# Performance work log

Hardware: AMD Instinct MI355X
Metric: run time of the kernel (lower is better)

The kernel has to match this reference:

```python
import jax, jax.numpy as jnp
import numpy as np
import math

N, C, H = 2048, 256, 8
D = C // H
T, R, E = 8, 12, 32768
BUCKETS = 21
SEED = 128


def _layernorm(x, g, b, eps=1e-5):
    mu = jnp.mean(x, axis=-1, keepdims=True)
    var = jnp.var(x, axis=-1, keepdims=True)
    return (x - mu) * jax.lax.rsqrt(var + eps) * g + b


def _bucketize_dt(dt, num_buckets):
    eps = 1e-06
    signed_log = jnp.sign(dt) * jnp.log1p(jnp.abs(dt) + eps)
    min_v, max_v = -5.0, 5.0
    norm = (jnp.clip(signed_log, min_v, max_v) - min_v) / (max_v - min_v + 1e-09)
    idx = jnp.floor(norm * (num_buckets - 1)).astype(jnp.int32)
    return jnp.clip(idx, 0, num_buckets - 1)


def setup_inputs() -> dict:
    key = jax.random.key(0)
    ks = jax.random.split(key, 24)
    s = 0.02
    inp = {
        'X': jax.random.normal(ks[0], (N, C), jnp.float32),
        'token_type': jax.random.randint(ks[1], (N,), 0, T, jnp.int32),
        'edge_src': jax.random.randint(ks[2], (E,), 0, N, jnp.int32),
        'edge_dst': jax.random.randint(ks[3], (E,), 0, N, jnp.int32),
        'edge_rel': jax.random.randint(ks[4], (E,), 0, R, jnp.int32),
        'time_vec': jax.random.normal(ks[5], (N,), jnp.float32),
        'seed_count': SEED,
        'Wq': jax.random.normal(ks[6], (C, C), jnp.float32) * s,
        'bq': jnp.zeros((C,), jnp.float32),
        'Wk': jax.random.normal(ks[7], (C, C), jnp.float32) * s,
        'bk': jnp.zeros((C,), jnp.float32),
        'Wv': jax.random.normal(ks[8], (C, C), jnp.float32) * s,
        'bv': jnp.zeros((C,), jnp.float32),
        'Wo': jax.random.normal(ks[9], (C, C), jnp.float32) * s,
        'bo': jnp.zeros((C,), jnp.float32),
        'ln1_g': jnp.ones((C,), jnp.float32),
        'ln1_b': jnp.zeros((C,), jnp.float32),
        'ln2_g': jnp.ones((C,), jnp.float32),
        'ln2_b': jnp.zeros((C,), jnp.float32),
        'W1': jax.random.normal(ks[10], (C, 4 * C), jnp.float32) * s,
        'b1': jnp.zeros((4 * C,), jnp.float32),
        'W2': jax.random.normal(ks[11], (4 * C, C), jnp.float32) * s,
        'b2': jnp.zeros((C,), jnp.float32),
        'adj_rel_bias': jnp.zeros((R, H), jnp.float32),
        'typepair_bias': jnp.zeros((T, T, H), jnp.float32),
        'temp_bias': jax.random.normal(ks[12], (BUCKETS, H), jnp.float32) * s,
    }
    return inp


def reference(X, token_type, edge_src, edge_dst, edge_rel, time_vec, seed_count,
              Wq, bq, Wk, bk, Wv, bv, Wo, bo,
              ln1_g, ln1_b, ln2_g, ln2_b, W1, b1, W2, b2,
              adj_rel_bias, typepair_bias, temp_bias):
    n = X.shape[0]
    h = _layernorm(X, ln1_g, ln1_b)
    q = (h @ Wq + bq).reshape(n, H, D)
    k = (h @ Wk + bk).reshape(n, H, D)
    v = (h @ Wv + bv).reshape(n, H, D)
    scores = jnp.einsum('nhd,mhd->hnm', q, k) / math.sqrt(D)  # [H, N, N]

    # structural bias, factored as [N, N, H] then transposed
    bias = typepair_bias[token_type][:, token_type]            # [N, N, H]
    bias = bias.at[edge_src, edge_dst].add(adj_rel_bias[edge_rel])
    # seed-wise temporal bias on the first seed_count rows
    dt = time_vec[None, :] - time_vec[:seed_count, None]       # [S, N]
    tb = temp_bias[_bucketize_dt(dt, BUCKETS)]                 # [S, N, H]
    bias = bias.at[:seed_count].add(tb)

    attn = jax.nn.softmax(scores + bias.transpose(2, 0, 1), axis=-1)
    o = jnp.einsum('hnm,mhd->nhd', attn, v).reshape(n, C)
    x = X + (o @ Wo + bo)

    h2 = _layernorm(x, ln2_g, ln2_b)
    f = jax.nn.gelu(h2 @ W1 + b1, approximate=False) @ W2 + b2
    return x + f
```

## Files before the change

### kernel.cpp

```cpp
#include <hip/hip_runtime.h>
#include <hip/hip_bf16.h>
#include <math.h>

#define NTOK 2048
#define CDIM 256
#define HHEADS 8
#define DHEAD 32
#define NEDGE 32768
#define NTILE 16
#define SPLITS 8
#define TPS 2
#define EXTD 64
#define LE 72

typedef __attribute__((ext_vector_type(8))) short short8;
typedef __attribute__((ext_vector_type(4))) short short4v;
typedef __attribute__((ext_vector_type(4))) float f32x4;

static __device__ inline short f2bf(float f) {
    __hip_bfloat16 h = __float2bfloat16(f);
    return *reinterpret_cast<short*>(&h);
}
static __device__ inline float bf2f(short s) {
    unsigned int u = ((unsigned int)(unsigned short)s) << 16;
    return *reinterpret_cast<float*>(&u);
}

__global__ __launch_bounds__(256) void ln4_kernel(const float* __restrict__ X,
    const float* __restrict__ g, const float* __restrict__ b, short* __restrict__ out)
{
    int t = threadIdx.x;
    int wv = t >> 6, lane = t & 63;
    int row = blockIdx.x * 4 + wv;

    float4 x = *(const float4*)&X[(size_t)row * CDIM + lane * 4];
    float s = x.x + x.y + x.z + x.w;
    #pragma unroll
    for (int off = 1; off < 64; off <<= 1) s += __shfl_xor(s, off);
    float mu = s * (1.0f / CDIM);
    float4 d = { x.x - mu, x.y - mu, x.z - mu, x.w - mu };
    float s2 = d.x * d.x + d.y * d.y + d.z * d.z + d.w * d.w;
    #pragma unroll
    for (int off = 1; off < 64; off <<= 1) s2 += __shfl_xor(s2, off);
    float rsig = rsqrtf(s2 * (1.0f / CDIM) + 1e-5f);
    float4 gg = *(const float4*)&g[lane * 4];
    float4 bb = *(const float4*)&b[lane * 4];
    short o4[4];
    o4[0] = f2bf(d.x * rsig * gg.x + bb.x);
    o4[1] = f2bf(d.y * rsig * gg.y + bb.y);
    o4[2] = f2bf(d.z * rsig * gg.z + bb.z);
    o4[3] = f2bf(d.w * rsig * gg.w + bb.w);
    *(short4v*)&out[(size_t)row * CDIM + lane * 4] = *(short4v*)o4;
}

static __device__ inline void transpose_tile_f32(const float* __restrict__ in,
    short* __restrict__ out, int K, int N, int k0, int n0, int t)
{
    __shared__ float tile[64][65];
    int r0 = t >> 4, c0 = (t & 15) * 4;
    #pragma unroll
    for (int i = 0; i < 4; i++) {
        int r = r0 + i * 16;
        float4 v = *(const float4*)(in + (size_t)(k0 + r) * N + n0 + c0);
        tile[r][c0 + 0] = v.x; tile[r][c0 + 1] = v.y;
        tile[r][c0 + 2] = v.z; tile[r][c0 + 3] = v.w;
    }
    __syncthreads();
    #pragma unroll
    for (int i = 0; i < 4; i++) {
        int nr = r0 + i * 16;
        short o4[4];
        #pragma unroll
        for (int j = 0; j < 4; j++) o4[j] = f2bf(tile[c0 + j][nr]);
        *(short4v*)(out + (size_t)(n0 + nr) * K + k0 + c0) = *(short4v*)o4;
    }
}

__global__ __launch_bounds__(256) void prep_kernel(
    const float* __restrict__ Wq, const float* __restrict__ Wk,
    const float* __restrict__ Wv, const float* __restrict__ Wo,
    const float* __restrict__ W1, const float* __restrict__ W2,
    short* __restrict__ wt_qkv, short* __restrict__ wot,
    short* __restrict__ w1t, short* __restrict__ w2t,
    const int* __restrict__ token_type, const float* __restrict__ typepair_bias,
    short* __restrict__ qh, short* __restrict__ kh,
    int* __restrict__ cnt2)
{
    int b = blockIdx.x;
    int t = threadIdx.x;
    if (b < 192) {
        const float* src; short* dst; int K, N, bx, by;
        if (b < 64) {
            int m = b >> 4, r = b & 15;
            src = (m == 0) ? Wq : (m == 1) ? Wk : (m == 2) ? Wv : Wo;
            dst = (m == 0) ? wt_qkv : (m == 1) ? wt_qkv + 256 * 256
                : (m == 2) ? wt_qkv + 512 * 256 : wot;
            K = 256; N = 256; bx = r & 3; by = r >> 2;
        } else if (b < 128) {
            int r = b - 64; src = W1; dst = w1t; K = 256; N = 1024; bx = r & 15; by = r >> 4;
        } else {
            int r = b - 128; src = W2; dst = w2t; K = 1024; N = 256; bx = r & 3; by = r >> 2;
        }
        transpose_tile_f32(src, dst, K, N, by * 64, bx * 64, t);
    } else if (b < 256) {
        int idx = (b - 192) * 256 + t;
        int row = idx >> 3, h = idx & 7;
        int tt = token_type[row];
        short qe[32], ke[32];
        #pragma unroll
        for (int j = 0; j < 32; j++) {
            if (j < 8) {
                qe[j] = f2bf(typepair_bias[(tt * 8 + j) * 8 + h]);
                ke[j] = (j == tt) ? (short)0x3F80 : (short)0;
            } else { qe[j] = 0; ke[j] = 0; }
        }
        size_t base = ((size_t)h * NTOK + row) * EXTD + 32;
        #pragma unroll
        for (int k = 0; k < 4; k++) {
            *(short8*)&qh[base + k * 8] = *(short8*)&qe[k * 8];
            *(short8*)&kh[base + k * 8] = *(short8*)&ke[k * 8];
        }
    } else {
        cnt2[(b - 256) * 256 + t] = 0;
        cnt2[(b - 256) * 256 + t + 8192] = 0;
        cnt2[(b - 256) * 256 + t + 16384] = 0;
        cnt2[(b - 256) * 256 + t + 24576] = 0;
    }
}

template<int EPI>
__global__ __launch_bounds__(256) void gemm32_kernel(
    const short* __restrict__ A, const short* __restrict__ Bt,
    const float* __restrict__ bias, const float* __restrict__ resid,
    void* __restrict__ out_, int M, int N, int K)
{
    __shared__ short A_lds[32 * 40];
    __shared__ short B_lds[64 * 40];

    const int t = threadIdx.x;
    const int w = t >> 6, lane = t & 63, c = lane & 15, g = lane >> 4;
    const int row0 = blockIdx.y * 32, col0 = blockIdx.x * 64;
    const int srow = t >> 2, sk = (t & 3) * 8;

    f32x4 acc[2] = {};

    for (int k0 = 0; k0 < K; k0 += 32) {
        if (t < 128)
            *(short8*)&A_lds[srow * 40 + sk] = *(const short8*)&A[(size_t)(row0 + srow) * K + k0 + sk];
        *(short8*)&B_lds[srow * 40 + sk] = *(const short8*)&Bt[(size_t)(col0 + srow) * K + k0 + sk];
        __syncthreads();
        short8 af = *(const short8*)&A_lds[((w & 1) * 16 + c) * 40 + g * 8];
        #pragma unroll
        for (int nf = 0; nf < 2; nf++) {
            short8 bf = *(const short8*)&B_lds[((w >> 1) * 32 + nf * 16 + c) * 40 + g * 8];
            acc[nf] = __builtin_amdgcn_mfma_f32_16x16x32_bf16(af, bf, acc[nf], 0, 0, 0);
        }
        __syncthreads();
    }

    #pragma unroll
    for (int nf = 0; nf < 2; nf++) {
        #pragma unroll
        for (int reg = 0; reg < 4; reg++) {
            int row = row0 + (w & 1) * 16 + g * 4 + reg;
            int col = col0 + (w >> 1) * 32 + nf * 16 + c;
            float v = acc[nf][reg] + bias[col];
            if (EPI == 2) {
                ((float*)out_)[(size_t)row * N + col] = v + resid[(size_t)row * N + col];
            } else {
                v = 0.5f * v * (1.0f + erff(v * 0.70710678118654752f));
                ((short*)out_)[(size_t)row * N + col] = f2bf(v);
            }
        }
    }
}

__global__ __launch_bounds__(256) void gemm32_qkv_kernel(
    const short* __restrict__ A, const short* __restrict__ Bt,
    const float* __restrict__ bq, const float* __restrict__ bk, const float* __restrict__ bv,
    short* __restrict__ qh, short* __restrict__ kh, short* __restrict__ vt)
{
    const int K = CDIM;
    __shared__ short A_lds[32 * 40];
    __shared__ short B_lds[64 * 40];

    const int t = threadIdx.x;
    const int w = t >> 6, lane = t & 63, c = lane & 15, g = lane >> 4;
    const int row0 = blockIdx.y * 32, col0 = blockIdx.x * 64;
    const int srow = t >> 2, sk = (t & 3) * 8;

    f32x4 acc[2] = {};

    for (int k0 = 0; k0 < K; k0 += 32) {
        if (t < 128)
            *(short8*)&A_lds[srow * 40 + sk] = *(const short8*)&A[(size_t)(row0 + srow) * K + k0 + sk];
        *(short8*)&B_lds[srow * 40 + sk] = *(const short8*)&Bt[(size_t)(col0 + srow) * K + k0 + sk];
        __syncthreads();
        short8 af = *(const short8*)&A_lds[((w & 1) * 16 + c) * 40 + g * 8];
        #pragma unroll
        for (int nf = 0; nf < 2; nf++) {
            short8 bf = *(const short8*)&B_lds[((w >> 1) * 32 + nf * 16 + c) * 40 + g * 8];
            acc[nf] = __builtin_amdgcn_mfma_f32_16x16x32_bf16(af, bf, acc[nf], 0, 0, 0);
        }
        __syncthreads();
    }

    const int region = col0 >> 8;
    const int colr0 = col0 & 255;
    const float* bias = (region == 0) ? bq : (region == 1) ? bk : bv;
    #pragma unroll
    for (int nf = 0; nf < 2; nf++) {
        #pragma unroll
        for (int reg = 0; reg < 4; reg++) {
            int row = row0 + (w & 1) * 16 + g * 4 + reg;
            int col = colr0 + (w >> 1) * 32 + nf * 16 + c;
            float v = acc[nf][reg] + bias[col];
            if (region == 0) v *= 0.17677669529663687f;
            short bb = f2bf(v);
            size_t hidx = ((size_t)(col >> 5) * NTOK + row) * EXTD + (col & 31);
            if (region == 0)      qh[hidx] = bb;
            else if (region == 1) kh[hidx] = bb;
            else                  vt[(size_t)col * NTOK + row] = bb;
        }
    }
}

__global__ void edge_hist2_kernel(const int* __restrict__ src, const int* __restrict__ dst,
    int* __restrict__ cnt, int E)
{
    int e = blockIdx.x * blockDim.x + threadIdx.x;
    if (e < E) atomicAdd(&cnt[src[e] * NTILE + (dst[e] >> 7)], 1);
}

__global__ __launch_bounds__(256) void edge_scan2_kernel(const int* __restrict__ cnt,
    int* __restrict__ row_ptr, int* __restrict__ wcur)
{
    __shared__ int sums[256];
    int t = threadIdx.x;
    int base = t * 128;
    int s = 0;
    for (int i = 0; i < 128; i++) s += cnt[base + i];
    sums[t] = s;
    __syncthreads();
    for (int off = 1; off < 256; off <<= 1) {
        int v = (t >= off) ? sums[t - off] : 0;
        __syncthreads();
        sums[t] += v;
        __syncthreads();
    }
    int run = (t == 0) ? 0 : sums[t - 1];
    for (int i = 0; i < 128; i++) {
        row_ptr[base + i] = run;
        wcur[base + i] = run;
        run += cnt[base + i];
    }
    if (t == 255) row_ptr[NTOK * NTILE] = run;
}

__global__ void edge_scatter2_kernel(const int* __restrict__ src, const int* __restrict__ dst,
    const int* __restrict__ rel, int* __restrict__ wcur, int2* __restrict__ pairs, int E)
{
    int e = blockIdx.x * blockDim.x + threadIdx.x;
    if (e < E) {
        int d = dst[e];
        int pos = atomicAdd(&wcur[src[e] * NTILE + (d >> 7)], 1);
        pairs[pos] = make_int2(d, rel[e]);
    }
}

#define QBLK 32
#define KBLK 128

__global__ __launch_bounds__(256) void attn_mfma3_kernel(
    const short* __restrict__ qh, const short* __restrict__ kh,
    const short* __restrict__ vt,
    const float* __restrict__ time_vec, const int* __restrict__ seed_ptr,
    const float* __restrict__ adj_rel_bias, const float* __restrict__ temp_bias,
    const int* __restrict__ row_ptr2, const int2* __restrict__ pairs2,
    float* __restrict__ Op_part, float2* __restrict__ ml_part)
{
    __shared__ __align__(16) short Q_lds[QBLK * LE];
    __shared__ __align__(16) short K_lds[KBLK * LE];
    __shared__ __align__(16) short Vt_lds[DHEAD * 136];
    __shared__ __align__(16) unsigned int P32[QBLK * 68];
    __shared__ float tcol_s[KBLK];
    __shared__ float temp_h[21];
    __shared__ float adj_h[12];
    __shared__ float2 ml[2][QBLK];

    const int h  = blockIdx.y;
    const int n0 = blockIdx.x * QBLK;
    const int sblk = blockIdx.z;
    const int t  = threadIdx.x;
    const int wv = t >> 6, lane = t & 63, c = lane & 15, g = lane >> 4;
    const int rowblk  = (wv & 1) * 16;
    const int halfIdx = wv >> 1;
    const int colhalf = halfIdx * 64;
    const int seed = seed_ptr[0];
    const bool blockTemporal = (n0 < seed);
    const int gt0 = sblk * TPS;

    {
        int row = t >> 3, off = (t & 7) * 8;
        *(short8*)&Q_lds[row * LE + off] =
            *(const short8*)&qh[((size_t)h * NTOK + n0 + row) * EXTD + off];
    }
    if (t < 21)  temp_h[t] = temp_bias[t * HHEADS + h];
    if (t < 12)  adj_h[t] = adj_rel_bias[t * HHEADS + h];

    const int nrow = n0 + rowblk + c;
    const bool rowTemporal = (nrow < seed);
    const float tn = time_vec[nrow];

    int2 rp01 = *(const int2*)&row_ptr2[nrow * NTILE + gt0];
    int  rp2  = row_ptr2[nrow * NTILE + gt0 + 2];

    const int krow = t >> 3, koff = (t & 7) * 8;
    const int vrow = t >> 4, voff = (t & 15) * 8;
    short8 kr0, kr1, kr2, kr3, vr0, vr1;
    float tcr = 0.0f;

    auto LOADT = [&](int gt) {
        int m0 = gt * KBLK;
        const short* kp = &kh[((size_t)h * NTOK + m0 + krow) * EXTD + koff];
        kr0 = *(const short8*)kp;
        kr1 = *(const short8*)(kp + (size_t)32 * EXTD);
        kr2 = *(const short8*)(kp + (size_t)64 * EXTD);
        kr3 = *(const short8*)(kp + (size_t)96 * EXTD);
        const short* vp = &vt[(size_t)(h * 32 + vrow) * NTOK + m0 + voff];
        vr0 = *(const short8*)vp;
        vr1 = *(const short8*)(vp + (size_t)16 * NTOK);
        if (blockTemporal && t < 128) tcr = time_vec[m0 + t];
    };
    auto WRITET = [&]() {
        *(short8*)&K_lds[krow * LE + koff]        = kr0;
        *(short8*)&K_lds[(krow + 32) * LE + koff] = kr1;
        *(short8*)&K_lds[(krow + 64) * LE + koff] = kr2;
        *(short8*)&K_lds[(krow + 96) * LE + koff] = kr3;
        *(short8*)&Vt_lds[vrow * 136 + voff]        = vr0;
        *(short8*)&Vt_lds[(vrow + 16) * 136 + voff] = vr1;
        if (blockTemporal && t < 128) tcol_s[t] = tcr;
    };

    float m_run = -INFINITY, l_run = 0.0f;
    f32x4 oacc[2] = {{0,0,0,0},{0,0,0,0}};
    const f32x4 zf = {0.0f, 0.0f, 0.0f, 0.0f};

    LOADT(gt0);
    WRITET();

    for (int tile = 0; tile < TPS; ++tile) {
        __syncthreads();
        if (tile + 1 < TPS) LOADT(gt0 + tile + 1);

        short8 qlo = *(const short8*)&Q_lds[(rowblk + c) * LE + g * 8];
        short8 qhi = *(const short8*)&Q_lds[(rowblk + c) * LE + 32 + g * 8];
        float vals[16];
        #pragma unroll
        for (int blk = 0; blk < 4; blk++) {
            const short* kb = &K_lds[(colhalf + blk * 16 + c) * LE];
            short8 klo = *(const short8*)(kb + g * 8);
            short8 khi = *(const short8*)(kb + 32 + g * 8);
            f32x4 acc = __builtin_amdgcn_mfma_f32_16x16x32_bf16(klo, qlo, zf, 0, 0, 0);
            acc = __builtin_amdgcn_mfma_f32_16x16x32_bf16(khi, qhi, acc, 0, 0, 0);
            #pragma unroll
            for (int reg = 0; reg < 4; reg++) vals[blk * 4 + reg] = acc[reg];
        }

        if (rowTemporal) {
            #pragma unroll
            for (int blk = 0; blk < 4; blk++) {
                #pragma unroll
                for (int reg = 0; reg < 4; reg++) {
                    float dt = tcol_s[colhalf + blk * 16 + g * 4 + reg] - tn;
                    float ab = fabsf(dt) + 1e-6f;
                    float sg = (dt > 0.0f) ? 1.0f : ((dt < 0.0f) ? -1.0f : 0.0f);
                    float sl = sg * log1pf(ab);
                    sl = fminf(fmaxf(sl, -5.0f), 5.0f);
                    float norm = (sl + 5.0f) * (1.0f / (10.0f + 1e-9f));
                    int bidx = (int)floorf(norm * 20.0f);
                    bidx = min(max(bidx, 0), 20);
                    vals[blk * 4 + reg] += temp_h[bidx];
                }
            }
        }
        {
            int e0 = (tile == 0) ? rp01.x : rp01.y;
            int e1 = (tile == 0) ? rp01.y : rp2;
            for (int e = e0; e < e1; ++e) {
                int2 pr = pairs2[e];
                int dloc = pr.x & 127;
                if ((dloc >> 6) == halfIdx) {
                    int ml64 = dloc & 63;
                    if (((ml64 >> 2) & 3) == g) {
                        float ab = adj_h[pr.y];
                        int li = (ml64 >> 4) * 4 + (ml64 & 3);
                        #pragma unroll
                        for (int i = 0; i < 16; i++) vals[i] += (i == li) ? ab : 0.0f;
                    }
                }
            }
        }

        float tmax = vals[0];
        #pragma unroll
        for (int i = 1; i < 16; i++) tmax = fmaxf(tmax, vals[i]);
        tmax = fmaxf(tmax, __shfl_xor(tmax, 16));
        tmax = fmaxf(tmax, __shfl_xor(tmax, 32));
        float m_new = fmaxf(m_run, tmax);
        float psum = 0.0f;
        #pragma unroll
        for (int i = 0; i < 16; i++) { vals[i] = __expf(vals[i] - m_new); psum += vals[i]; }
        psum += __shfl_xor(psum, 16);
        psum += __shfl_xor(psum, 32);
        float scale = __expf(m_run - m_new);
        m_run = m_new;
        l_run = l_run * scale + psum;

        #pragma unroll
        for (int blk = 0; blk < 4; blk++) {
            #pragma unroll
            for (int r = 0; r < 2; r++) {
                unsigned lo = (unsigned short)f2bf(vals[blk * 4 + 2 * r]);
                unsigned hi = (unsigned short)f2bf(vals[blk * 4 + 2 * r + 1]);
                P32[(rowblk + c) * 68 + halfIdx * 32 + blk * 8 + g * 2 + r] = lo | (hi << 16);
            }
        }

        float scr[4];
        #pragma unroll
        for (int reg = 0; reg < 4; reg++) scr[reg] = __shfl(scale, 4 * g + reg);
        #pragma unroll
        for (int dblk = 0; dblk < 2; dblk++)
            #pragma unroll
            for (int reg = 0; reg < 4; reg++) oacc[dblk][reg] *= scr[reg];
        #pragma unroll
        for (int kc = 0; kc < 2; kc++) {
            short8 pa = *(const short8*)&P32[(rowblk + c) * 68 + halfIdx * 32 + kc * 16 + g * 4];
            #pragma unroll
            for (int dblk = 0; dblk < 2; dblk++) {
                short8 vb = *(const short8*)&Vt_lds[(dblk * 16 + c) * 136 + colhalf + kc * 32 + g * 8];
                oacc[dblk] = __builtin_amdgcn_mfma_f32_16x16x32_bf16(pa, vb, oacc[dblk], 0, 0, 0);
            }
        }

        __syncthreads();
        if (tile + 1 < TPS) WRITET();
    }

    __syncthreads();
    if (lane < 16) ml[halfIdx][rowblk + lane] = make_float2(m_run, l_run);
    __syncthreads();

    float* Op = (float*)K_lds;
    #pragma unroll
    for (int reg = 0; reg < 4; reg++) {
        int rw = rowblk + 4 * g + reg;
        float2 a0 = ml[0][rw], a1 = ml[1][rw];
        float mm = fmaxf(a0.x, a1.x);
        float wh = __expf((halfIdx == 0 ? a0.x : a1.x) - mm);
        Op[halfIdx * 32 * 36 + rw * 36 + c]      = oacc[0][reg] * wh;
        Op[halfIdx * 32 * 36 + rw * 36 + 16 + c] = oacc[1][reg] * wh;
    }
    __syncthreads();

    {
        int row = t >> 3, d0 = (t & 7) * 4;
        float2 a0 = ml[0][row], a1 = ml[1][row];
        float mm = fmaxf(a0.x, a1.x);
        float w0 = __expf(a0.x - mm), w1 = __expf(a1.x - mm);
        float lc = a0.y * w0 + a1.y * w1;
        float4 pa = *(const float4*)&Op[row * 36 + d0];
        float4 pb = *(const float4*)&Op[(32 + row) * 36 + d0];
        float4 sum;
        sum.x = pa.x + pb.x; sum.y = pa.y + pb.y;
        sum.z = pa.z + pb.z; sum.w = pa.w + pb.w;
        *(float4*)&Op_part[((size_t)sblk * NTOK + n0 + row) * CDIM + h * DHEAD + d0] = sum;
        if ((t & 7) == 0)
            ml_part[((size_t)sblk * NTOK + n0 + row) * HHEADS + h] = make_float2(mm, lc);
    }
}

__global__ __launch_bounds__(256) void attn_reduce_kernel(
    const float* __restrict__ Op_part, const float2* __restrict__ ml_part,
    short* __restrict__ o)
{
    int row = blockIdx.x;
    int t = threadIdx.x;
    int h = t >> 5, d = t & 31;

    float2 a[SPLITS];
    float mm = -INFINITY;
    #pragma unroll
    for (int s = 0; s < SPLITS; s++) {
        a[s] = ml_part[((size_t)s * NTOK + row) * HHEADS + h];
        mm = fmaxf(mm, a[s].x);
    }
    float l = 0.0f, w[SPLITS];
    #pragma unroll
    for (int s = 0; s < SPLITS; s++) { w[s] = __expf(a[s].x - mm); l += a[s].y * w[s]; }
    float inv = 1.0f / l;
    size_t idx = (size_t)row * CDIM + h * DHEAD + d;
    float acc = 0.0f;
    #pragma unroll
    for (int s = 0; s < SPLITS; s++)
        acc += w[s] * Op_part[(size_t)s * NTOK * CDIM + idx];
    o[idx] = f2bf(acc * inv);
}

extern "C" void kernel_launch(void* const* d_in, const int* in_sizes, int n_in,
                              void* d_out, int out_size, void* d_ws, size_t ws_size,
                              hipStream_t stream)
{
    (void)in_sizes; (void)n_in; (void)out_size; (void)ws_size;
    const float* X        = (const float*)d_in[0];
    const int* token_type = (const int*)d_in[1];
    const int* edge_src   = (const int*)d_in[2];
    const int* edge_dst   = (const int*)d_in[3];
    const int* edge_rel   = (const int*)d_in[4];
    const float* time_vec = (const float*)d_in[5];
    const int* seed_ptr   = (const int*)d_in[6];
    const float* Wq = (const float*)d_in[7];  const float* bq = (const float*)d_in[8];
    const float* Wk = (const float*)d_in[9];  const float* bk = (const float*)d_in[10];
    const float* Wv = (const float*)d_in[11]; const float* bv = (const float*)d_in[12];
    const float* Wo = (const float*)d_in[13]; const float* bo = (const float*)d_in[14];
    const float* ln1_g = (const float*)d_in[15]; const float* ln1_b = (const float*)d_in[16];
    const float* ln2_g = (const float*)d_in[17]; const float* ln2_b = (const float*)d_in[18];
    const float* W1 = (const float*)d_in[19]; const float* b1 = (const float*)d_in[20];
    const float* W2 = (const float*)d_in[21]; const float* b2 = (const float*)d_in[22];
    const float* adj_rel_bias  = (const float*)d_in[23];
    const float* typepair_bias = (const float*)d_in[24];
    const float* temp_bias     = (const float*)d_in[25];
    float* out = (float*)d_out;

    char* base = (char*)d_ws;
    size_t off = 0;
    auto alloc = [&](size_t bytes) { char* p = base + off; off += (bytes + 255) & ~(size_t)255; return p; };
    short* qh_bf   = (short*)alloc((size_t)HHEADS * NTOK * EXTD * 2);
    short* kh_bf   = (short*)alloc((size_t)HHEADS * NTOK * EXTD * 2);
    short* vt_bf   = (short*)alloc((size_t)256 * NTOK * 2);
    short* h1_bf   = (short*)alloc((size_t)NTOK * 256 * 2);
    short* h2_bf   = (short*)alloc((size_t)NTOK * 256 * 2);
    short* o_bf    = (short*)alloc((size_t)NTOK * 256 * 2);
    short* mid_bf  = (short*)alloc((size_t)NTOK * 1024 * 2);
    float* xb      = (float*)alloc((size_t)NTOK * 256 * 4);
    short* wt_qkv  = (short*)alloc((size_t)768 * 256 * 2);
    short* wot     = (short*)alloc((size_t)256 * 256 * 2);
    short* w1t     = (short*)alloc((size_t)1024 * 256 * 2);
    short* w2t     = (short*)alloc((size_t)256 * 1024 * 2);
    int2*  pairs2  = (int2*)alloc((size_t)NEDGE * 8);
    int*   cnt2    = (int*)alloc((size_t)NTOK * NTILE * 4);
    int*   rowptr2 = (int*)alloc(((size_t)NTOK * NTILE + 1) * 4);
    int*   wcur2   = (int*)alloc((size_t)NTOK * NTILE * 4);
    float* Op_part = (float*)alloc((size_t)SPLITS * NTOK * CDIM * 4);
    float2* ml_part = (float2*)alloc((size_t)SPLITS * NTOK * HHEADS * 8);

    prep_kernel<<<288, 256, 0, stream>>>(Wq, Wk, Wv, Wo, W1, W2,
                                         wt_qkv, wot, w1t, w2t,
                                         token_type, typepair_bias,
                                         qh_bf, kh_bf, cnt2);

    edge_hist2_kernel<<<NEDGE / 256, 256, 0, stream>>>(edge_src, edge_dst, cnt2, NEDGE);
    edge_scan2_kernel<<<1, 256, 0, stream>>>(cnt2, rowptr2, wcur2);
    edge_scatter2_kernel<<<NEDGE / 256, 256, 0, stream>>>(edge_src, edge_dst, edge_rel, wcur2, pairs2, NEDGE);

    ln4_kernel<<<NTOK / 4, 256, 0, stream>>>(X, ln1_g, ln1_b, h1_bf);

    gemm32_qkv_kernel<<<dim3(12, 64), 256, 0, stream>>>(h1_bf, wt_qkv, bq, bk, bv,
                                                        qh_bf, kh_bf, vt_bf);

    attn_mfma3_kernel<<<dim3(NTOK / QBLK, HHEADS, SPLITS), 256, 0, stream>>>(
        qh_bf, kh_bf, vt_bf, time_vec, seed_ptr,
        adj_rel_bias, temp_bias, rowptr2, pairs2, Op_part, ml_part);
    attn_reduce_kernel<<<NTOK, 256, 0, stream>>>(Op_part, ml_part, o_bf);

    gemm32_kernel<2><<<dim3(4, 64), 256, 0, stream>>>(o_bf, wot, bo, X, xb, NTOK, 256, 256);

    ln4_kernel<<<NTOK / 4, 256, 0, stream>>>(xb, ln2_g, ln2_b, h2_bf);

    gemm32_kernel<3><<<dim3(16, 64), 256, 0, stream>>>(h2_bf, w1t, b1, nullptr, mid_bf, NTOK, 1024, 256);
    gemm32_kernel<2><<<dim3(4, 64), 256, 0, stream>>>(mid_bf, w2t, b2, xb, out, NTOK, 256, 1024);
}
```

Baseline: 169.3 us.

## Materialize full attention score matrix and split attention into GEMM, softmax, PV kernels

When the workspace is large enough, the fused split-K flash-style attention is replaced by three kernels. The first writes the full bf16 score matrix per head to global memory. The second adds the temporal and edge biases and applies a row softmax in place. The third multiplies the probabilities by V. This drops the online-softmax rescaling and the partial-output reduction pass, but adds roughly 64 MB of score traffic written and read twice, and stores scores and probabilities in bf16. The old fused path stays as a fallback when the workspace is too small.

```diff
diff --git a/kernel.cpp b/kernel.cpp
--- a/kernel.cpp
+++ b/kernel.cpp
@@ -265,6 +265,175 @@
         int d = dst[e];
         int pos = atomicAdd(&wcur[src[e] * NTILE + (d >> 7)], 1);
         pairs[pos] = make_int2(d, rel[e]);
+    }
+}
+
+__global__ __launch_bounds__(256) void sgemm_kernel(
+    const short* __restrict__ qh, const short* __restrict__ kh,
+    short* __restrict__ S)
+{
+    __shared__ short A_lds[64 * LE];
+    __shared__ short B_lds[64 * LE];
+    const int t = threadIdx.x;
+    const int w = t >> 6, lane = t & 63, c = lane & 15, g = lane >> 4;
+    const int h = blockIdx.z;
+    const int m0 = blockIdx.x * 64, n0 = blockIdx.y * 64;
+
+    {
+        int r = t >> 3, off = (t & 7) * 8;
+        *(short8*)&A_lds[r * LE + off] =
+            *(const short8*)&qh[((size_t)h * NTOK + n0 + r) * EXTD + off];
+        *(short8*)&A_lds[(r + 32) * LE + off] =
+            *(const short8*)&qh[((size_t)h * NTOK + n0 + 32 + r) * EXTD + off];
+        *(short8*)&B_lds[r * LE + off] =
+            *(const short8*)&kh[((size_t)h * NTOK + m0 + r) * EXTD + off];
+        *(short8*)&B_lds[(r + 32) * LE + off] =
+            *(const short8*)&kh[((size_t)h * NTOK + m0 + 32 + r) * EXTD + off];
+    }
+    __syncthreads();
+
+    short8 alo = *(const short8*)&A_lds[(w * 16 + c) * LE + g * 8];
+    short8 ahi = *(const short8*)&A_lds[(w * 16 + c) * LE + 32 + g * 8];
+    f32x4 acc[4] = {};
+    #pragma unroll
+    for (int nf = 0; nf < 4; nf++) {
+        short8 blo = *(const short8*)&B_lds[(nf * 16 + c) * LE + g * 8];
+        short8 bhi = *(const short8*)&B_lds[(nf * 16 + c) * LE + 32 + g * 8];
+        acc[nf] = __builtin_amdgcn_mfma_f32_16x16x32_bf16(alo, blo, acc[nf], 0, 0, 0);
+        acc[nf] = __builtin_amdgcn_mfma_f32_16x16x32_bf16(ahi, bhi, acc[nf], 0, 0, 0);
+    }
+
+    #pragma unroll
+    for (int nf = 0; nf < 4; nf++)
+        #pragma unroll
+        for (int reg = 0; reg < 4; reg++) {
+            int row = n0 + w * 16 + g * 4 + reg;
+            int col = m0 + nf * 16 + c;
+            S[((size_t)h * NTOK + row) * NTOK + col] = f2bf(acc[nf][reg]);
+        }
+}
+
+__global__ __launch_bounds__(256) void softmax_kernel(
+    short* __restrict__ S,
+    const float* __restrict__ time_vec, const int* __restrict__ seed_ptr,
+    const float* __restrict__ adj_rel_bias, const float* __restrict__ temp_bias,
+    const int* __restrict__ row_ptr2, const int2* __restrict__ pairs2)
+{
+    __shared__ float rowbuf[4][NTOK];
+
+    int t = threadIdx.x, wv = t >> 6, lane = t & 63;
+    int task = blockIdx.x * 4 + wv;
+    int h = task >> 11, n = task & 2047;
+    int seed = seed_ptr[0];
+    bool temporal = (n < seed);
+    float tn = time_vec[n];
+    float* rb = rowbuf[wv];
+    short* Srow = &S[((size_t)h * NTOK + n) * NTOK];
+
+    #pragma unroll
+    for (int i = 0; i < 4; i++) {
+        int m0 = i * 512 + lane * 8;
+        short8 sv = *(const short8*)&Srow[m0];
+        float v[8];
+        #pragma unroll
+        for (int j = 0; j < 8; j++) v[j] = bf2f(sv[j]);
+        if (temporal) {
+            float4 ta = *(const float4*)&time_vec[m0];
+            float4 tb = *(const float4*)&time_vec[m0 + 4];
+            float tv8[8] = { ta.x, ta.y, ta.z, ta.w, tb.x, tb.y, tb.z, tb.w };
+            #pragma unroll
+            for (int j = 0; j < 8; j++) {
+                float dt = tv8[j] - tn;
+                float ab = fabsf(dt) + 1e-6f;
+                float sg = (dt > 0.0f) ? 1.0f : ((dt < 0.0f) ? -1.0f : 0.0f);
+                float sl = sg * log1pf(ab);
+                sl = fminf(fmaxf(sl, -5.0f), 5.0f);
+                float norm = (sl + 5.0f) * (1.0f / (10.0f + 1e-9f));
+                int bidx = (int)floorf(norm * 20.0f);
+                bidx = min(max(bidx, 0), 20);
+                v[j] += temp_bias[bidx * 8 + h];
+            }
+        }
+        float4 lo = { v[0], v[1], v[2], v[3] };
+        float4 hi = { v[4], v[5], v[6], v[7] };
+        *(float4*)&rb[m0] = lo;
+        *(float4*)&rb[m0 + 4] = hi;
+    }
+    __syncthreads();
+
+    {
+        int e0 = row_ptr2[n * NTILE], e1 = row_ptr2[(n + 1) * NTILE];
+        for (int e = e0 + lane; e < e1; e += 64) {
+            int2 pr = pairs2[e];
+            atomicAdd(&rb[pr.x], adj_rel_bias[pr.y * 8 + h]);
+        }
+    }
+    __syncthreads();
+
+    float vv[32];
+    float mx = -INFINITY;
+    #pragma unroll
+    for (int i = 0; i < 4; i++) {
+        float4 a = *(const float4*)&rb[i * 512 + lane * 8];
+        float4 b = *(const float4*)&rb[i * 512 + lane * 8 + 4];
+        vv[i * 8 + 0] = a.x; vv[i * 8 + 1] = a.y; vv[i * 8 + 2] = a.z; vv[i * 8 + 3] = a.w;
+        vv[i * 8 + 4] = b.x; vv[i * 8 + 5] = b.y; vv[i * 8 + 6] = b.z; vv[i * 8 + 7] = b.w;
+    }
+    #pragma unroll
+    for (int i = 0; i < 32; i++) mx = fmaxf(mx, vv[i]);
+    #pragma unroll
+    for (int off = 1; off < 64; off <<= 1) mx = fmaxf(mx, __shfl_xor(mx, off));
+    float sum = 0.0f;
+    #pragma unroll
+    for (int i = 0; i < 32; i++) { vv[i] = __expf(vv[i] - mx); sum += vv[i]; }
+    #pragma unroll
+    for (int off = 1; off < 64; off <<= 1) sum += __shfl_xor(sum, off);
+    float inv = 1.0f / sum;
+
+    #pragma unroll
+    for (int i = 0; i < 4; i++) {
+        short p8[8];
+        #pragma unroll
+        for (int j = 0; j < 8; j++) p8[j] = f2bf(vv[i * 8 + j] * inv);
+        *(short8*)&Srow[i * 512 + lane * 8] = *(short8*)p8;
+    }
+}
+
+__global__ __launch_bounds__(256) void pv_kernel(
+    const short* __restrict__ P, const short* __restrict__ vt,
+    short* __restrict__ o)
+{
+    __shared__ short A_lds[32 * LE];
+    __shared__ short B_lds[32 * LE];
+    const int t = threadIdx.x;
+    const int w = t >> 6, lane = t & 63, c = lane & 15, g = lane >> 4;
+    const int h = blockIdx.y;
+    const int n0 = blockIdx.x * 32;
+    const int rowblk = (w & 1) * 16, colblk = (w >> 1) * 16;
+
+    f32x4 acc = {0.0f, 0.0f, 0.0f, 0.0f};
+
+    for (int k0 = 0; k0 < NTOK; k0 += 64) {
+        int r = t >> 3, off = (t & 7) * 8;
+        *(short8*)&A_lds[r * LE + off] =
+            *(const short8*)&P[((size_t)h * NTOK + n0 + r) * NTOK + k0 + off];
+        *(short8*)&B_lds[r * LE + off] =
+            *(const short8*)&vt[(size_t)(h * 32 + r) * NTOK + k0 + off];
+        __syncthreads();
+        short8 alo = *(const short8*)&A_lds[(rowblk + c) * LE + g * 8];
+        short8 ahi = *(const short8*)&A_lds[(rowblk + c) * LE + 32 + g * 8];
+        short8 blo = *(const short8*)&B_lds[(colblk + c) * LE + g * 8];
+        short8 bhi = *(const short8*)&B_lds[(colblk + c) * LE + 32 + g * 8];
+        acc = __builtin_amdgcn_mfma_f32_16x16x32_bf16(alo, blo, acc, 0, 0, 0);
+        acc = __builtin_amdgcn_mfma_f32_16x16x32_bf16(ahi, bhi, acc, 0, 0, 0);
+        __syncthreads();
+    }
+
+    #pragma unroll
+    for (int reg = 0; reg < 4; reg++) {
+        int row = n0 + rowblk + g * 4 + reg;
+        int col = h * 32 + colblk + c;
+        o[(size_t)row * CDIM + col] = f2bf(acc[reg]);
     }
 }
 
@@ -512,7 +681,7 @@
                               void* d_out, int out_size, void* d_ws, size_t ws_size,
                               hipStream_t stream)
 {
-    (void)in_sizes; (void)n_in; (void)out_size; (void)ws_size;
+    (void)in_sizes; (void)n_in; (void)out_size;
     const float* X        = (const float*)d_in[0];
     const int* token_type = (const int*)d_in[1];
     const int* edge_src   = (const int*)d_in[2];
@@ -552,27 +721,36 @@
     int*   cnt2    = (int*)alloc((size_t)NTOK * NTILE * 4);
     int*   rowptr2 = (int*)alloc(((size_t)NTOK * NTILE + 1) * 4);
     int*   wcur2   = (int*)alloc((size_t)NTOK * NTILE * 4);
-    float* Op_part = (float*)alloc((size_t)SPLITS * NTOK * CDIM * 4);
-    float2* ml_part = (float2*)alloc((size_t)SPLITS * NTOK * HHEADS * 8);
+
+    const size_t s_bytes = (size_t)HHEADS * NTOK * NTOK * 2;
+    const bool bigws = (ws_size >= off + s_bytes + (1u << 20));
 
     prep_kernel<<<288, 256, 0, stream>>>(Wq, Wk, Wv, Wo, W1, W2,
                                          wt_qkv, wot, w1t, w2t,
                                          token_type, typepair_bias,
                                          qh_bf, kh_bf, cnt2);
-
     edge_hist2_kernel<<<NEDGE / 256, 256, 0, stream>>>(edge_src, edge_dst, cnt2, NEDGE);
     edge_scan2_kernel<<<1, 256, 0, stream>>>(cnt2, rowptr2, wcur2);
     edge_scatter2_kernel<<<NEDGE / 256, 256, 0, stream>>>(edge_src, edge_dst, edge_rel, wcur2, pairs2, NEDGE);
 
     ln4_kernel<<<NTOK / 4, 256, 0, stream>>>(X, ln1_g, ln1_b, h1_bf);
-
     gemm32_qkv_kernel<<<dim3(12, 64), 256, 0, stream>>>(h1_bf, wt_qkv, bq, bk, bv,
                                                         qh_bf, kh_bf, vt_bf);
 
-    attn_mfma3_kernel<<<dim3(NTOK / QBLK, HHEADS, SPLITS), 256, 0, stream>>>(
-        qh_bf, kh_bf, vt_bf, time_vec, seed_ptr,
-        adj_rel_bias, temp_bias, rowptr2, pairs2, Op_part, ml_part);
-    attn_reduce_kernel<<<NTOK, 256, 0, stream>>>(Op_part, ml_part, o_bf);
+    if (bigws) {
+        short* S = (short*)alloc(s_bytes);
+        sgemm_kernel<<<dim3(32, 32, 8), 256, 0, stream>>>(qh_bf, kh_bf, S);
+        softmax_kernel<<<NTOK * HHEADS / 4, 256, 0, stream>>>(
+            S, time_vec, seed_ptr, adj_rel_bias, temp_bias, rowptr2, pairs2);
+        pv_kernel<<<dim3(64, 8), 256, 0, stream>>>(S, vt_bf, o_bf);
+    } else {
+        float* Op_part  = (float*)alloc((size_t)SPLITS * NTOK * CDIM * 4);
+        float2* ml_part = (float2*)alloc((size_t)SPLITS * NTOK * HHEADS * 8);
+        attn_mfma3_kernel<<<dim3(NTOK / QBLK, HHEADS, SPLITS), 256, 0, stream>>>(
+            qh_bf, kh_bf, vt_bf, time_vec, seed_ptr,
+            adj_rel_bias, temp_bias, rowptr2, pairs2, Op_part, ml_part);
+        attn_reduce_kernel<<<NTOK, 256, 0, stream>>>(Op_part, ml_part, o_bf);
+    }
 
     gemm32_kernel<2><<<dim3(4, 64), 256, 0, stream>>>(o_bf, wot, bo, X, xb, NTOK, 256, 256);
 
```

New measurement: 151.9 us. -10.3%, faster.
